# Performance work log

Measured on AMD Instinct MI355X. Metric: run time of the kernel, lower is better.

The kernel has to match this reference:

```python
import jax, jax.numpy as jnp
import numpy as np

N, M, K = 131072, 64, 8


def setup_inputs() -> dict:
    key = jax.random.key(0)
    k1, k2, k3, k4 = jax.random.split(key, 4)
    return {
        "H_real": jax.random.normal(k1, (N, M, K), dtype=jnp.float32),
        "H_imag": jax.random.normal(k2, (N, M, K), dtype=jnp.float32),
        "V_real": jax.random.normal(k3, (N, M, K), dtype=jnp.float32),
        "V_imag": jax.random.normal(k4, (N, M, K), dtype=jnp.float32),
        "noise_power": jnp.ones((1,), dtype=jnp.float32),
    }


def reference(H_real, H_imag, V_real, V_imag, noise_power):
    # Cross-products of all (user k1, beam k2) pairs in two batched matmuls.
    # real/imag parts of h_{k1}^T v_{k2} (no conjugate, matching the torch code)
    real_part = jnp.einsum('nmk,nml->nkl', H_real, V_real) - jnp.einsum('nmk,nml->nkl', H_imag, V_imag)  # (N,K,K)
    imag_part = jnp.einsum('nmk,nml->nkl', H_real, V_imag) + jnp.einsum('nmk,nml->nkl', H_imag, V_real)  # (N,K,K)
    norm2 = real_part ** 2 + imag_part ** 2  # (N,K,K): |h_{k1}^T v_{k2}|^2
    nom = jnp.diagonal(norm2, axis1=1, axis2=2)              # (N,K) signal power
    denom = norm2.sum(axis=2) - nom + noise_power            # (N,K) interference + noise
    rate = jnp.log2(1.0 + nom / denom)                       # (N,K)
    loss = -jnp.mean(jnp.sum(rate, axis=1))
    return loss
```

## Files before the change

### kernel.cpp

```cpp
#include <hip/hip_runtime.h>
#include <cstdint>
#include <cmath>

#define N_TOT 131072
#define NBLK  1024
#define WPB   4
#define ITERS (N_TOT / (NBLK * WPB))

__global__ __launch_bounds__(256, 4)
void srl_main(const float* __restrict__ Hr, const float* __restrict__ Hi,
              const float* __restrict__ Vr, const float* __restrict__ Vi,
              const float* __restrict__ noise_p, float* __restrict__ partials) {
  __shared__ float buf[WPB][4][512];
  __shared__ float red[WPB];

  const int tid  = threadIdx.x;
  const int w    = tid >> 6;
  const int lane = tid & 63;
  const int k    = lane >> 3;
  const int l    = lane & 7;
  const float noise = noise_p[0];

  float* b0 = buf[w][0];
  float* b1 = buf[w][1];
  float* b2 = buf[w][2];
  float* b3 = buf[w][3];

  float acc = 0.f;
  const int n0 = blockIdx.x * (ITERS * WPB) + w;

  for (int it = 0; it < ITERS; ++it) {
    const size_t base = (size_t)(n0 + it * WPB) * 512;
    const float4* gh_r = (const float4*)(Hr + base);
    const float4* gh_i = (const float4*)(Hi + base);
    const float4* gv_r = (const float4*)(Vr + base);
    const float4* gv_i = (const float4*)(Vi + base);

    ((float4*)b0)[lane]      = gh_r[lane];
    ((float4*)b0)[64 + lane] = gh_r[64 + lane];
    ((float4*)b1)[lane]      = gh_i[lane];
    ((float4*)b1)[64 + lane] = gh_i[64 + lane];
    ((float4*)b2)[lane]      = gv_r[lane];
    ((float4*)b2)[64 + lane] = gv_r[64 + lane];
    ((float4*)b3)[lane]      = gv_i[lane];
    ((float4*)b3)[64 + lane] = gv_i[64 + lane];
    asm volatile("s_waitcnt lgkmcnt(0)" ::: "memory");

    float re0 = 0.f, im0 = 0.f, re1 = 0.f, im1 = 0.f;
#pragma unroll
    for (int m = 0; m < 64; m += 2) {
      const float hr0 = b0[m * 8 + k];
      const float hi0 = b1[m * 8 + k];
      const float vr0 = b2[m * 8 + l];
      const float vi0 = b3[m * 8 + l];
      const float hr1 = b0[(m + 1) * 8 + k];
      const float hi1 = b1[(m + 1) * 8 + k];
      const float vr1 = b2[(m + 1) * 8 + l];
      const float vi1 = b3[(m + 1) * 8 + l];
      re0 = fmaf(hr0, vr0, re0); re0 = fmaf(-hi0, vi0, re0);
      im0 = fmaf(hr0, vi0, im0); im0 = fmaf(hi0, vr0, im0);
      re1 = fmaf(hr1, vr1, re1); re1 = fmaf(-hi1, vi1, re1);
      im1 = fmaf(hr1, vi1, im1); im1 = fmaf(hi1, vr1, im1);
    }
    asm volatile("s_waitcnt lgkmcnt(0)" ::: "memory");

    const float re  = re0 + re1;
    const float im  = im0 + im1;
    const float nrm = fmaf(re, re, im * im);

    float s = nrm;
    s += __shfl_xor(s, 1);
    s += __shfl_xor(s, 2);
    s += __shfl_xor(s, 4);

    if (l == k) {
      const float denom = (s - nrm) + noise;
      acc += log2f(1.f + nrm / denom);
    }
    asm volatile("s_waitcnt lgkmcnt(0)" ::: "memory");
  }

#pragma unroll
  for (int off = 1; off < 64; off <<= 1) acc += __shfl_xor(acc, off);
  if (lane == 0) red[w] = acc;
  __syncthreads();
  if (tid == 0) partials[blockIdx.x] = red[0] + red[1] + red[2] + red[3];
}

__global__ __launch_bounds__(256)
void srl_finalize(const float* __restrict__ partials, float* __restrict__ out) {
  const int tid = threadIdx.x;
  float a = 0.f;
#pragma unroll
  for (int i = 0; i < NBLK / 256; ++i) a += partials[tid + i * 256];
#pragma unroll
  for (int off = 1; off < 64; off <<= 1) a += __shfl_xor(a, off);
  __shared__ float r[4];
  if ((tid & 63) == 0) r[tid >> 6] = a;
  __syncthreads();
  if (tid == 0) out[0] = -(r[0] + r[1] + r[2] + r[3]) * (1.f / (float)N_TOT);
}

extern "C" void kernel_launch(void* const* d_in, const int* in_sizes, int n_in,
                              void* d_out, int out_size, void* d_ws, size_t ws_size,
                              hipStream_t stream) {
  const float* Hr = (const float*)d_in[0];
  const float* Hi = (const float*)d_in[1];
  const float* Vr = (const float*)d_in[2];
  const float* Vi = (const float*)d_in[3];
  const float* nz = (const float*)d_in[4];
  float* out      = (float*)d_out;
  float* partials = (float*)d_ws;

  srl_main<<<NBLK, 256, 0, stream>>>(Hr, Hi, Vr, Vi, nz, partials);
  srl_finalize<<<1, 256, 0, stream>>>(partials, out);
}
```

Before: 813.2 us.

## Use FP64 MFMA for complex cross-products and direct global-to-LDS loads

```diff
diff --git a/kernel.cpp b/kernel.cpp
--- a/kernel.cpp
+++ b/kernel.cpp
@@ -7,77 +7,85 @@
 #define WPB   4
 #define ITERS (N_TOT / (NBLK * WPB))
 
+typedef double f64x4 __attribute__((ext_vector_type(4)));
+
+__device__ __forceinline__ void gld_lds16(const float* g, float* l) {
+  __builtin_amdgcn_global_load_lds(
+      (const __attribute__((address_space(1))) void*)g,
+      (__attribute__((address_space(3))) void*)l, 16, 0, 0);
+}
+
 __global__ __launch_bounds__(256, 4)
 void srl_main(const float* __restrict__ Hr, const float* __restrict__ Hi,
               const float* __restrict__ Vr, const float* __restrict__ Vi,
               const float* __restrict__ noise_p, float* __restrict__ partials) {
-  __shared__ float buf[WPB][4][512];
+  __shared__ float buf[WPB][2048];
   __shared__ float red[WPB];
 
   const int tid  = threadIdx.x;
   const int w    = tid >> 6;
   const int lane = tid & 63;
-  const int k    = lane >> 3;
-  const int l    = lane & 7;
+  const int c    = lane & 15;
+  const int hi   = lane >> 4;
+  const int c7   = c & 7;
+  const int sel  = c >> 3;
   const float noise = noise_p[0];
 
-  float* b0 = buf[w][0];
-  float* b1 = buf[w][1];
-  float* b2 = buf[w][2];
-  float* b3 = buf[w][3];
+  float* base = buf[w];
+  const int rbase = sel * 512 + hi * 8 + c7;
 
   float acc = 0.f;
   const int n0 = blockIdx.x * (ITERS * WPB) + w;
 
   for (int it = 0; it < ITERS; ++it) {
-    const size_t base = (size_t)(n0 + it * WPB) * 512;
-    const float4* gh_r = (const float4*)(Hr + base);
-    const float4* gh_i = (const float4*)(Hi + base);
-    const float4* gv_r = (const float4*)(Vr + base);
-    const float4* gv_i = (const float4*)(Vi + base);
+    const size_t gbase = (size_t)(n0 + it * WPB) * 512 + (size_t)(lane * 4);
 
-    ((float4*)b0)[lane]      = gh_r[lane];
-    ((float4*)b0)[64 + lane] = gh_r[64 + lane];
-    ((float4*)b1)[lane]      = gh_i[lane];
-    ((float4*)b1)[64 + lane] = gh_i[64 + lane];
-    ((float4*)b2)[lane]      = gv_r[lane];
-    ((float4*)b2)[64 + lane] = gv_r[64 + lane];
-    ((float4*)b3)[lane]      = gv_i[lane];
-    ((float4*)b3)[64 + lane] = gv_i[64 + lane];
     asm volatile("s_waitcnt lgkmcnt(0)" ::: "memory");
+    gld_lds16(Hr + gbase,       base);
+    gld_lds16(Hr + gbase + 256, base + 256);
+    gld_lds16(Hi + gbase,       base + 512);
+    gld_lds16(Hi + gbase + 256, base + 768);
+    gld_lds16(Vr + gbase,       base + 1024);
+    gld_lds16(Vr + gbase + 256, base + 1280);
+    gld_lds16(Vi + gbase,       base + 1536);
+    gld_lds16(Vi + gbase + 256, base + 1792);
+    asm volatile("s_waitcnt vmcnt(0)" ::: "memory");
 
-    float re0 = 0.f, im0 = 0.f, re1 = 0.f, im1 = 0.f;
+    f64x4 a0 = {0., 0., 0., 0.}, a1 = {0., 0., 0., 0.};
 #pragma unroll
-    for (int m = 0; m < 64; m += 2) {
-      const float hr0 = b0[m * 8 + k];
-      const float hi0 = b1[m * 8 + k];
-      const float vr0 = b2[m * 8 + l];
-      const float vi0 = b3[m * 8 + l];
-      const float hr1 = b0[(m + 1) * 8 + k];
-      const float hi1 = b1[(m + 1) * 8 + k];
-      const float vr1 = b2[(m + 1) * 8 + l];
-      const float vi1 = b3[(m + 1) * 8 + l];
-      re0 = fmaf(hr0, vr0, re0); re0 = fmaf(-hi0, vi0, re0);
-      im0 = fmaf(hr0, vi0, im0); im0 = fmaf(hi0, vr0, im0);
-      re1 = fmaf(hr1, vr1, re1); re1 = fmaf(-hi1, vi1, re1);
-      im1 = fmaf(hr1, vi1, im1); im1 = fmaf(hi1, vr1, im1);
+    for (int t = 0; t < 16; t += 2) {
+      const double xa0 = (double)base[rbase + 32 * t];
+      const double xb0 = (double)base[1024 + rbase + 32 * t];
+      const double xa1 = (double)base[rbase + 32 * (t + 1)];
+      const double xb1 = (double)base[1024 + rbase + 32 * (t + 1)];
+      a0 = __builtin_amdgcn_mfma_f64_16x16x4f64(xa0, xb0, a0, 0, 0, 0);
+      a1 = __builtin_amdgcn_mfma_f64_16x16x4f64(xa1, xb1, a1, 0, 0, 0);
     }
-    asm volatile("s_waitcnt lgkmcnt(0)" ::: "memory");
 
-    const float re  = re0 + re1;
-    const float im  = im0 + im1;
-    const float nrm = fmaf(re, re, im * im);
-
-    float s = nrm;
-    s += __shfl_xor(s, 1);
-    s += __shfl_xor(s, 2);
-    s += __shfl_xor(s, 4);
-
-    if (l == k) {
-      const float denom = (s - nrm) + noise;
-      acc += log2f(1.f + nrm / denom);
+    float nrm[4], nomv[4];
+#pragma unroll
+    for (int v = 0; v < 4; ++v) {
+      const float cf  = (float)(a0[v] + a1[v]);
+      const float x8  = __shfl_xor(cf, 8);
+      const float x32 = __shfl_xor(cf, 32);
+      const float x40 = __shfl_xor(cf, 40);
+      const float re  = cf - x40;
+      const float im  = x8 + x32;
+      nrm[v]  = fmaf(re, re, im * im);
+      nomv[v] = nrm[v];
     }
-    asm volatile("s_waitcnt lgkmcnt(0)" ::: "memory");
+#pragma unroll
+    for (int v = 0; v < 4; ++v) {
+      nrm[v] += __shfl_xor(nrm[v], 1);
+      nrm[v] += __shfl_xor(nrm[v], 2);
+      nrm[v] += __shfl_xor(nrm[v], 4);
+    }
+    if (hi < 2 && (c >> 2) == hi) {
+      const int   v     = c & 3;
+      const float nom   = nomv[v];
+      const float denom = (nrm[v] - nom) + noise;
+      acc += log2f(1.f + nom / denom);
+    }
   }
 
 #pragma unroll
```

After: 806.8 us. About the same (-0.8%).
